# Performance work log

Measured on AMD Instinct MI355X. Metric: run time of the kernel, lower is better.

## Reference

```python
import jax, jax.numpy as jnp
import numpy as np

N_TRAIN, N_TEST, D = 8192, 4096, 16


def setup_inputs() -> dict:
    key = jax.random.key(0)
    k1, k2, k3, k4 = jax.random.split(key, 4)
    train_x = jax.random.normal(k1, (N_TRAIN, D), dtype=jnp.float32)
    train_y = jax.random.normal(k2, (N_TRAIN,), dtype=jnp.float32)
    x = jax.random.normal(k3, (N_TEST, D), dtype=jnp.float32)
    # trained hyperparameters (positive): ScaleKernel outputscale, ARD lengthscales, likelihood noise
    outputscale = jnp.array([0.8], dtype=jnp.float32)
    lengthscale = jax.random.uniform(k4, (D,), dtype=jnp.float32, minval=0.5, maxval=1.5)
    noise = jnp.array([0.05], dtype=jnp.float32)
    return {"train_x": train_x, "train_y": train_y, "x": x,
            "outputscale": outputscale, "lengthscale": lengthscale, "noise": noise}


def _rbf(x1, x2, lengthscale, outputscale):
    # ScaleKernel(RBFKernel(ard)): k(a,b) = s * exp(-0.5 * sum_d ((a_d-b_d)/l_d)^2)
    a = x1 / lengthscale
    b = x2 / lengthscale
    d2 = (jnp.sum(a * a, axis=-1)[:, None]
          + jnp.sum(b * b, axis=-1)[None, :]
          - 2.0 * a @ b.T)
    return outputscale * jnp.exp(-0.5 * jnp.maximum(d2, 0.0))


def reference(train_x, train_y, x, outputscale, lengthscale, noise):
    s = outputscale[0]
    sn = noise[0]
    n = train_x.shape[0]
    # Exact GP posterior with zero mean + Gaussian likelihood:
    # Kxx_hat = K(X,X) + sn*I ; mean = Kxs^T Kxx_hat^{-1} y
    Kxx = _rbf(train_x, train_x, lengthscale, s) + sn * jnp.eye(n, dtype=train_x.dtype)
    L = jnp.linalg.cholesky(Kxx)                       # [N,N]
    Kxs = _rbf(train_x, x, lengthscale, s)             # [N,M]
    alpha = jax.scipy.linalg.cho_solve((L, True), train_y)
    mean = Kxs.T @ alpha                               # [M]
    # predictive variance diag: k(x,x)=s ; var = s - ||L^{-1} Kxs||^2 + noise (likelihood)
    v = jax.scipy.linalg.solve_triangular(L, Kxs, lower=True)  # [N,M]
    var = s - jnp.sum(v * v, axis=0) + sn              # [M]
    return mean, var
```

## Files before the change

### kernel.cpp

```cpp
#include <hip/hip_runtime.h>
#include <stdint.h>


#define N_TRAIN 8192
#define N_TEST  4096
#define DIM     16
#define KDIM    8192
#define CG_ITERS 4
#define NT      (KDIM / 64)

using f32x4  = __attribute__((ext_vector_type(4))) float;
using bf16x8 = __attribute__((ext_vector_type(8))) short;

static __device__ __forceinline__ unsigned short f2bf(float f) {
  unsigned u = __float_as_uint(f);
  u = (u + 0x7FFFu + ((u >> 16) & 1u)) >> 16;
  return (unsigned short)u;
}
static __device__ __forceinline__ float bf2f(unsigned short h) {
  return __uint_as_float(((unsigned)h) << 16);
}

__device__ __forceinline__ void gl_lds16(const void* g, void* l) {
  __builtin_amdgcn_global_load_lds(
      (const __attribute__((address_space(1))) unsigned int*)g,
      (__attribute__((address_space(3))) unsigned int*)l, 16, 0, 0);
}

template <int N>
__device__ __forceinline__ void block_reduceN(float* v, float* sbuf) {
  #pragma unroll
  for (int off = 32; off > 0; off >>= 1)
    #pragma unroll
    for (int i = 0; i < N; ++i) v[i] += __shfl_down(v[i], off);
  int lane = threadIdx.x & 63, w = threadIdx.x >> 6;
  if (lane == 0)
    #pragma unroll
    for (int i = 0; i < N; ++i) sbuf[w * N + i] = v[i];
  __syncthreads();
  #pragma unroll
  for (int i = 0; i < N; ++i)
    v[i] = sbuf[i] + sbuf[N + i] + sbuf[2 * N + i] + sbuf[3 * N + i];
}

__global__ void prep_kernel(const float* __restrict__ tx, const float* __restrict__ xx,
                            const float* __restrict__ ls,
                            float* __restrict__ As, float* __restrict__ an,
                            float* __restrict__ Bs, float* __restrict__ bn) {
  int i = blockIdx.x * 256 + threadIdx.x;
  if (i < N_TRAIN) {
    float s = 0.f;
    #pragma unroll
    for (int d = 0; d < DIM; ++d) {
      float v = tx[(size_t)i * DIM + d] / ls[d];
      As[(size_t)i * DIM + d] = v; s += v * v;
    }
    an[i] = s;
  } else if (i < N_TRAIN + N_TEST) {
    int j = i - N_TRAIN;
    float s = 0.f;
    #pragma unroll
    for (int d = 0; d < DIM; ++d) {
      float v = xx[(size_t)j * DIM + d] / ls[d];
      Bs[(size_t)j * DIM + d] = v; s += v * v;
    }
    bn[j] = s;
  }
}

template <bool DIAG0>
__global__ __launch_bounds__(256) void build_kernel(
    const float* __restrict__ RI, const float* __restrict__ nI,
    const float* __restrict__ RJ, const float* __restrict__ nJ,
    unsigned short* __restrict__ O1,
    const float* __restrict__ osc)
{
  __shared__ float aI[128 * DIM];
  __shared__ float sI[128];
  int t = threadIdx.x;
  int j0 = blockIdx.x * 512, i0 = blockIdx.y * 128;
  for (int e = t; e < 128 * DIM; e += 256) aI[e] = RI[(size_t)i0 * DIM + e];
  if (t < 128) sI[t] = nI[i0 + t];
  __syncthreads();

  int ja = j0 + 2 * t, jb = ja + 1;
  f32x4 aj0[4], aj1[4];
  const f32x4* RJa = (const f32x4*)(RJ + (size_t)ja * DIM);
  const f32x4* RJb = (const f32x4*)(RJ + (size_t)jb * DIM);
  #pragma unroll
  for (int q = 0; q < 4; ++q) { aj0[q] = RJa[q]; aj1[q] = RJb[q]; }
  float nja = nJ[ja], njb = nJ[jb];
  float s = osc[0];

  for (int ic = 0; ic < 128; ic += 2) {
    f32x4 rv[2][4];
    #pragma unroll
    for (int r = 0; r < 2; ++r)
      #pragma unroll
      for (int q = 0; q < 4; ++q)
        rv[r][q] = *(const f32x4*)&aI[(ic + r) * DIM + q * 4];
    #pragma unroll
    for (int r = 0; r < 2; ++r) {
      int i = ic + r;
      float d0 = 0.f, d1 = 0.f;
      #pragma unroll
      for (int q = 0; q < 4; ++q) {
        f32x4 ai = rv[r][q];
        d0 += ai[0]*aj0[q][0] + ai[1]*aj0[q][1] + ai[2]*aj0[q][2] + ai[3]*aj0[q][3];
        d1 += ai[0]*aj1[q][0] + ai[1]*aj1[q][1] + ai[2]*aj1[q][2] + ai[3]*aj1[q][3];
      }
      float d2a = fmaxf(sI[i] + nja - 2.f * d0, 0.f);
      float d2b = fmaxf(sI[i] + njb - 2.f * d1, 0.f);
      float va = s * __expf(-0.5f * d2a);
      float vb = s * __expf(-0.5f * d2b);
      if (DIAG0 && (i0 + i == ja)) va = 0.f;
      if (DIAG0 && (i0 + i == jb)) vb = 0.f;
      unsigned pack = (unsigned)f2bf(va) | ((unsigned)f2bf(vb) << 16);
      *(unsigned*)&O1[(size_t)(i0 + i) * KDIM + ja] = pack;
    }
  }
}


__device__ __forceinline__ void stage_h(const char* gtile, int kbyte,
                                        char* ldsdst, int tid, int wave) {
  #pragma unroll
  for (int q = 0; q < 2; ++q) {
    int o = q * 8192 + tid * 16;
    int r = o >> 7;
    int c = (o & 127) ^ ((r & 7) << 4);
    gl_lds16(gtile + (size_t)r * (KDIM * 2) + kbyte + c,
             ldsdst + q * 8192 + wave * 1024);
  }
}

template <int FINAL>
__global__ __launch_bounds__(512, 1) void gemm256(
    const unsigned short* __restrict__ A,
    const unsigned short* __restrict__ Bm,
    unsigned short* __restrict__ Cq,
    int gy, float* __restrict__ pq)
{
  __shared__ char Ab[2][2][16384];
  __shared__ char Bb[2][2][16384];
  const int tid = threadIdx.x, lane = tid & 63, wave = tid >> 6;
  const int wm = wave >> 2, wn = wave & 3;
  const int nwg = gridDim.x, orig = blockIdx.x;
  const int wgid = (orig & 7) * (nwg >> 3) + (orig >> 3);
  const int bx = wgid / gy, by = wgid % gy;
  const size_t HALF = (size_t)128 * KDIM * 2;

  const char* bA = (const char*)(A  + (size_t)(by * 256) * KDIM);
  const char* bB = (const char*)(Bm + (size_t)(bx * 256) * KDIM);

  const int ar = wm * 64 + (lane & 15);
  const int br = wn * 32 + (lane & 15);
  const int hi = (lane >> 4) * 16;
  int aoff[4][2], boff[2][2];
  #pragma unroll
  for (int mf = 0; mf < 4; ++mf)
    #pragma unroll
    for (int kk = 0; kk < 2; ++kk)
      aoff[mf][kk] = (ar + mf * 16) * 128 + ((hi + kk * 64) ^ ((ar & 7) << 4));
  #pragma unroll
  for (int nf = 0; nf < 2; ++nf)
    #pragma unroll
    for (int kk = 0; kk < 2; ++kk)
      boff[nf][kk] = (br + nf * 16) * 128 + ((hi + kk * 64) ^ ((br & 7) << 4));

  f32x4 acc[2][2][4][2] = {};
  bf16x8 aR[4][2], bR[2][2][2];

#define BAR() __builtin_amdgcn_s_barrier()
#define PRIO1 __builtin_amdgcn_s_setprio(1)
#define PRIO0 __builtin_amdgcn_s_setprio(0)
#define FENCE8() asm volatile("s_waitcnt vmcnt(8)" ::: "memory")
#define FENCE6() asm volatile("s_waitcnt vmcnt(6)" ::: "memory")
#define FENCE0() asm volatile("s_waitcnt vmcnt(0)" ::: "memory")
#define STAGE_A(buf, mh, kb) stage_h(bA + ((mh) ? HALF : 0), kb, &Ab[buf][mh][0], tid, wave)
#define STAGE_B(buf, mh, kb) stage_h(bB + ((mh) ? HALF : 0), kb, &Bb[buf][mh][0], tid, wave)
#define LOAD_A(buf, mh)                                                        \
  { _Pragma("unroll") for (int mf = 0; mf < 4; ++mf)                           \
      _Pragma("unroll") for (int kk = 0; kk < 2; ++kk)                         \
        aR[mf][kk] = *(const bf16x8*)(&Ab[buf][mh][0] + aoff[mf][kk]); }
#define LOAD_B(buf, nh)                                                        \
  { _Pragma("unroll") for (int nf = 0; nf < 2; ++nf)                           \
      _Pragma("unroll") for (int kk = 0; kk < 2; ++kk)                         \
        bR[nh][nf][kk] = *(const bf16x8*)(&Bb[buf][nh][0] + boff[nf][kk]); }
#define MFMA16(mh, nh)                                                         \
  { _Pragma("unroll") for (int kk = 0; kk < 2; ++kk)                           \
      _Pragma("unroll") for (int mf = 0; mf < 4; ++mf)                         \
        _Pragma("unroll") for (int nf = 0; nf < 2; ++nf)                       \
          acc[mh][nh][mf][nf] = __builtin_amdgcn_mfma_f32_16x16x32_bf16(       \
              aR[mf][kk], bR[nh][nf][kk], acc[mh][nh][mf][nf], 0, 0, 0); }

  STAGE_A(0, 0, 0);   STAGE_B(0, 0, 0);   STAGE_B(0, 1, 0);   STAGE_A(0, 1, 0);
  STAGE_A(1, 0, 128); STAGE_B(1, 0, 128); STAGE_B(1, 1, 128); STAGE_A(1, 1, 128);
  FENCE6();
  BAR();

  for (int t = 0; t < NT; t += 2) {
    const bool g = (t + 2 < NT);
    const int kb2 = (t + 2) * 128, kb3 = (t + 3) * 128;
    LOAD_A(0, 0); LOAD_B(0, 0);
    BAR(); PRIO1; MFMA16(0, 0); PRIO0; BAR();
    if (g) STAGE_A(0, 0, kb2);
    LOAD_B(0, 1);
    BAR(); PRIO1; MFMA16(0, 1); PRIO0; BAR();
    if (g) STAGE_B(0, 0, kb2);
    LOAD_A(0, 1);
    BAR(); PRIO1; MFMA16(1, 0); PRIO0; BAR();
    if (g) { STAGE_B(0, 1, kb2); STAGE_A(0, 1, kb2); }
    BAR(); PRIO1; MFMA16(1, 1); PRIO0;
    if (g) { FENCE8(); } else { FENCE0(); }
    BAR();
    LOAD_A(1, 0); LOAD_B(1, 0);
    BAR(); PRIO1; MFMA16(0, 0); PRIO0; BAR();
    if (g) STAGE_A(1, 0, kb3);
    LOAD_B(1, 1);
    BAR(); PRIO1; MFMA16(0, 1); PRIO0; BAR();
    if (g) STAGE_B(1, 0, kb3);
    LOAD_A(1, 1);
    BAR(); PRIO1; MFMA16(1, 0); PRIO0; BAR();
    if (g) { STAGE_B(1, 1, kb3); STAGE_A(1, 1, kb3); }
    BAR(); PRIO1; MFMA16(1, 1); PRIO0;
    if (g) { FENCE6(); }
    BAR();
  }

  const int bm = by * 256, bn = bx * 256;
  if (!FINAL) {
    #pragma unroll
    for (int mh = 0; mh < 2; ++mh)
      #pragma unroll
      for (int nh = 0; nh < 2; ++nh)
        #pragma unroll
        for (int mf = 0; mf < 4; ++mf)
          #pragma unroll
          for (int nf = 0; nf < 2; ++nf) {
            int row = bm + mh * 128 + wm * 64 + mf * 16 + (lane >> 4) * 4;
            int col = bn + nh * 128 + wn * 32 + nf * 16 + (lane & 15);
            #pragma unroll
            for (int rg = 0; rg < 4; ++rg)
              Cq[(size_t)(row + rg) * KDIM + col] = f2bf(acc[mh][nh][mf][nf][rg]);
          }
  } else {
    #pragma unroll
    for (int mh = 0; mh < 2; ++mh)
      #pragma unroll
      for (int mf = 0; mf < 4; ++mf)
        #pragma unroll
        for (int rg = 0; rg < 4; ++rg) {
          int row = bm + mh * 128 + wm * 64 + mf * 16 + (lane >> 4) * 4 + rg;
          float v = 0.f;
          #pragma unroll
          for (int nh = 0; nh < 2; ++nh)
            #pragma unroll
            for (int nf = 0; nf < 2; ++nf) {
              int col = bn + nh * 128 + wn * 32 + nf * 16 + (lane & 15);
              v += acc[mh][nh][mf][nf][rg] * bf2f(A[(size_t)row * KDIM + col]);
            }
          v += __shfl_xor(v, 1); v += __shfl_xor(v, 2);
          v += __shfl_xor(v, 4); v += __shfl_xor(v, 8);
          if ((lane & 15) == 0) atomicAdd(&pq[row], v);
        }
  }
#undef MFMA16
#undef LOAD_B
#undef LOAD_A
#undef STAGE_B
#undef STAGE_A
#undef FENCE0
#undef FENCE6
#undef FENCE8
#undef PRIO0
#undef PRIO1
#undef BAR
}

template <bool FIRST>
__global__ __launch_bounds__(256) void cg_step(
    const unsigned short* __restrict__ Q, unsigned short* __restrict__ R,
    unsigned short* __restrict__ P, const float* __restrict__ y,
    float* __restrict__ scal, float* __restrict__ pq,
    const float* __restrict__ osc, const float* __restrict__ noi)
{
  __shared__ float sbuf[24];
  int c = blockIdx.x, t = threadIdx.x;
  size_t base = (size_t)c * KDIM;
  float dg = osc[0] + noi[0];

  bf16x8 q8[4], r8[4], p8[4];
  #pragma unroll
  for (int k = 0; k < 4; ++k) q8[k] = *(const bf16x8*)&Q[base + k * 2048 + t * 8];
  #pragma unroll
  for (int k = 0; k < 4; ++k) r8[k] = *(const bf16x8*)&R[base + k * 2048 + t * 8];
  if (FIRST) {
    #pragma unroll
    for (int k = 0; k < 4; ++k) p8[k] = r8[k];
  } else {
    #pragma unroll
    for (int k = 0; k < 4; ++k) p8[k] = *(const bf16x8*)&P[base + k * 2048 + t * 8];
  }

  float v[6] = {0.f, 0.f, 0.f, 0.f, 0.f, 0.f};
  #pragma unroll
  for (int k = 0; k < 4; ++k) {
    int j = k * 2048 + t * 8;
    f32x4 ya = *(const f32x4*)&y[j];
    f32x4 yb = *(const f32x4*)&y[j + 4];
    #pragma unroll
    for (int e = 0; e < 8; ++e) {
      float qv = bf2f((unsigned short)q8[k][e]);
      float rv = bf2f((unsigned short)r8[k][e]);
      float yv = (e < 4) ? ya[e] : yb[e - 4];
      if (FIRST) {
        v[0] += rv * qv; v[1] += qv * qv; v[2] += yv * qv;
        v[3] += rv * rv; v[4] += yv * rv;
      } else {
        float pv = bf2f((unsigned short)p8[k][e]);
        v[0] += pv * qv; v[1] += rv * qv; v[2] += qv * qv; v[3] += yv * qv;
        v[4] += pv * pv; v[5] += rv * pv;
      }
    }
  }
  block_reduceN<6>(v, sbuf);

  float rr, yp, yr, mean, bx;
  float pq_od, rq_od, qq_od, yq_od, pp, rp;
  if (FIRST) {
    rr = v[3]; yp = v[4]; yr = v[4]; mean = 0.f; bx = 0.f;
    pq_od = v[0]; rq_od = v[0]; qq_od = v[1]; yq_od = v[2];
    pp = v[3]; rp = v[3];
  } else {
    rr = scal[c*8+0]; yp = scal[c*8+1]; yr = scal[c*8+2];
    mean = scal[c*8+3]; bx = scal[c*8+4];
    pq_od = v[0]; rq_od = v[1]; qq_od = v[2]; yq_od = v[3];
    pp = v[4]; rp = v[5];
  }
  float pAp   = pq_od + dg * pp;
  float rq_e  = rq_od + dg * rp;
  float qq_e  = qq_od + 2.f * dg * pq_od + dg * dg * pp;
  float yq_e  = yq_od + dg * yp;

  float alpha = rr / fmaxf(pAp, 1e-30f);
  mean += alpha * yp;
  bx   += alpha * rr;
  float rrn = fmaxf(rr - 2.f * alpha * rq_e + alpha * alpha * qq_e, 0.f);
  float yrn = yr - alpha * yq_e;
  float beta = rrn / fmaxf(rr, 1e-30f);
  float ypn  = yrn + beta * yp;

  float spp = 0.f;
  #pragma unroll
  for (int k = 0; k < 4; ++k) {
    int j = k * 2048 + t * 8;
    bf16x8 wr, wp;
    #pragma unroll
    for (int e = 0; e < 8; ++e) {
      float pv = bf2f((unsigned short)p8[k][e]);
      float qe = bf2f((unsigned short)q8[k][e]) + dg * pv;
      float rn = bf2f((unsigned short)r8[k][e]) - alpha * qe;
      unsigned short hb = f2bf(rn);
      wr[e] = (short)hb;
      unsigned short hp = f2bf(bf2f(hb) + beta * pv);
      wp[e] = (short)hp;
      float ppv = bf2f(hp);
      spp += ppv * ppv;
    }
    *(bf16x8*)&R[base + j] = wr;
    *(bf16x8*)&P[base + j] = wp;
  }
  __syncthreads();
  float vv[1] = {spp};
  block_reduceN<1>(vv, sbuf);

  if (t == 0) {
    scal[c*8+0] = rrn; scal[c*8+1] = ypn; scal[c*8+2] = yrn;
    scal[c*8+3] = mean; scal[c*8+4] = bx; scal[c*8+5] = vv[0];
    pq[c] = 0.f;
  }
}

__global__ void final_out(float* __restrict__ pq, const float* __restrict__ scal,
                          const float* __restrict__ osc, const float* __restrict__ noi,
                          float* __restrict__ out, int c0, int C)
{
  int c = blockIdx.x * 256 + threadIdx.x;
  if (c >= C) return;
  float dg = osc[0] + noi[0];
  float rr = scal[c*8+0], yp = scal[c*8+1];
  float mean = scal[c*8+3], bx = scal[c*8+4], pp = scal[c*8+5];
  float pAp = pq[c] + dg * pp;
  float alpha = rr / fmaxf(pAp, 1e-30f);
  mean += alpha * yp;
  bx   += alpha * rr;
  out[c0 + c] = mean;
  out[N_TEST + c0 + c] = dg - bx;
  pq[c] = 0.f;
}

extern "C" void kernel_launch(void* const* d_in, const int* in_sizes, int n_in,
                              void* d_out, int out_size, void* d_ws, size_t ws_size,
                              hipStream_t stream) {
  const float* tx = (const float*)d_in[0];
  const float* ty = (const float*)d_in[1];
  const float* xx = (const float*)d_in[2];
  const float* os = (const float*)d_in[3];
  const float* ls = (const float*)d_in[4];
  const float* ns = (const float*)d_in[5];
  float* out = (float*)d_out;
  (void)in_sizes; (void)n_in; (void)out_size;

  auto pad = [](size_t x) { return (x + 255) & ~(size_t)255; };
  size_t fixed = pad((size_t)N_TRAIN * KDIM * 2)
               + pad((size_t)N_TRAIN * DIM * 4) + pad((size_t)N_TRAIN * 4)
               + pad((size_t)N_TEST * DIM * 4) + pad((size_t)N_TEST * 4);
  int C = 4096;
  while (C > 256) {
    size_t tot = fixed + 3 * pad((size_t)C * KDIM * 2)
               + pad((size_t)C * 32) + pad((size_t)C * 4);
    if (tot <= ws_size) break;
    C >>= 1;
  }

  char* w = (char*)d_ws;
  auto alloc = [&](size_t bytes) { char* p = w; w += ((bytes + 255) & ~(size_t)255); return p; };
  unsigned short* Kb = (unsigned short*)alloc((size_t)N_TRAIN * KDIM * 2);
  float* As = (float*)alloc((size_t)N_TRAIN * DIM * 4);
  float* an = (float*)alloc((size_t)N_TRAIN * 4);
  float* Bs = (float*)alloc((size_t)N_TEST * DIM * 4);
  float* bn = (float*)alloc((size_t)N_TEST * 4);
  unsigned short* Rb = (unsigned short*)alloc((size_t)C * KDIM * 2);
  unsigned short* Pb = (unsigned short*)alloc((size_t)C * KDIM * 2);
  unsigned short* Qb = (unsigned short*)alloc((size_t)C * KDIM * 2);
  float* scal = (float*)alloc((size_t)C * 32);
  float* pq   = (float*)alloc((size_t)C * 4);

  prep_kernel<<<48, 256, 0, stream>>>(tx, xx, ls, As, an, Bs, bn);

  build_kernel<true><<<dim3(KDIM / 512, N_TRAIN / 128), 256, 0, stream>>>(
      As, an, As, an, Kb, os);

  for (int c0 = 0; c0 < N_TEST; c0 += C) {
    build_kernel<false><<<dim3(KDIM / 512, C / 128), 256, 0, stream>>>(
        Bs + (size_t)c0 * DIM, bn + c0, As, an, Rb, os);
    int gy = C / 256;
    dim3 gg(32 * gy);
    int scb = (C + 255) / 256;
    for (int it = 0; it < CG_ITERS; ++it) {
      const unsigned short* Ain = (it == 0) ? Rb : Pb;
      int fin = (it == CG_ITERS - 1) ? 1 : 0;
      if (!fin) {
        gemm256<0><<<gg, 512, 0, stream>>>(Ain, Kb, Qb, gy, pq);
        if (it == 0)
          cg_step<true><<<C, 256, 0, stream>>>(Qb, Rb, Pb, ty, scal, pq, os, ns);
        else
          cg_step<false><<<C, 256, 0, stream>>>(Qb, Rb, Pb, ty, scal, pq, os, ns);
      } else {
        gemm256<1><<<gg, 512, 0, stream>>>(Ain, Kb, Qb, gy, pq);
        final_out<<<scb, 256, 0, stream>>>(pq, scal, os, ns, out, c0, C);
      }
    }
  }
}
```

Measured before the change: 1.981 ms.

## Build RBF kernel matrices with bf16 split-precision MFMA and LDS-staged stores

Replaces the scalar FP32 dot-product build kernel with an MFMA version. Each scaled input is split into bf16 hi/lo parts packed so that two 16x16x32 MFMAs approximate the FP32 cross product to about hi*hi+hi*lo+lo*hi accuracy. Results go through an LDS tile and are written out as coalesced 16-byte rows. This targets the cost of building the 8192x8192 and 8192xC kernel matrices. The trade-off is extra prep buffers and slightly reduced dot-product precision.

```diff
diff --git a/kernel.cpp b/kernel.cpp
--- a/kernel.cpp
+++ b/kernel.cpp
@@ -45,15 +45,24 @@
 
 __global__ void prep_kernel(const float* __restrict__ tx, const float* __restrict__ xx,
                             const float* __restrict__ ls,
-                            float* __restrict__ As, float* __restrict__ an,
-                            float* __restrict__ Bs, float* __restrict__ bn) {
+                            unsigned short* __restrict__ TPK,
+                            unsigned short* __restrict__ THH,
+                            unsigned short* __restrict__ TLL,
+                            float* __restrict__ an,
+                            unsigned short* __restrict__ XPK,
+                            float* __restrict__ bn) {
   int i = blockIdx.x * 256 + threadIdx.x;
   if (i < N_TRAIN) {
     float s = 0.f;
     #pragma unroll
     for (int d = 0; d < DIM; ++d) {
       float v = tx[(size_t)i * DIM + d] / ls[d];
-      As[(size_t)i * DIM + d] = v; s += v * v;
+      s += v * v;
+      unsigned short hi = f2bf(v);
+      unsigned short lo = f2bf(v - bf2f(hi));
+      TPK[(size_t)i * 32 + d] = hi;  TPK[(size_t)i * 32 + 16 + d] = lo;
+      THH[(size_t)i * 32 + d] = hi;  THH[(size_t)i * 32 + 16 + d] = hi;
+      TLL[(size_t)i * 32 + d] = lo;  TLL[(size_t)i * 32 + 16 + d] = lo;
     }
     an[i] = s;
   } else if (i < N_TRAIN + N_TEST) {
@@ -62,65 +71,74 @@
     #pragma unroll
     for (int d = 0; d < DIM; ++d) {
       float v = xx[(size_t)j * DIM + d] / ls[d];
-      Bs[(size_t)j * DIM + d] = v; s += v * v;
+      s += v * v;
+      unsigned short hi = f2bf(v);
+      unsigned short lo = f2bf(v - bf2f(hi));
+      XPK[(size_t)j * 32 + d] = hi;  XPK[(size_t)j * 32 + 16 + d] = lo;
     }
     bn[j] = s;
   }
 }
 
+#define TLDS 136
+
 template <bool DIAG0>
-__global__ __launch_bounds__(256) void build_kernel(
-    const float* __restrict__ RI, const float* __restrict__ nI,
-    const float* __restrict__ RJ, const float* __restrict__ nJ,
-    unsigned short* __restrict__ O1,
+__global__ __launch_bounds__(256) void build_mfma(
+    const unsigned short* __restrict__ IPK,
+    const float* __restrict__ nI,
+    const unsigned short* __restrict__ JHH,
+    const unsigned short* __restrict__ JLL,
+    const float* __restrict__ nJ,
+    unsigned short* __restrict__ O,
     const float* __restrict__ osc)
 {
-  __shared__ float aI[128 * DIM];
-  __shared__ float sI[128];
-  int t = threadIdx.x;
-  int j0 = blockIdx.x * 512, i0 = blockIdx.y * 128;
-  for (int e = t; e < 128 * DIM; e += 256) aI[e] = RI[(size_t)i0 * DIM + e];
+  __shared__ unsigned short tile[128 * TLDS];
+  __shared__ float sI[128], sJ[128];
+  int t = threadIdx.x, lane = t & 63, wave = t >> 6;
+  int i0 = blockIdx.y * 128, j0 = blockIdx.x * 128;
   if (t < 128) sI[t] = nI[i0 + t];
+  else         sJ[t - 128] = nJ[j0 + t - 128];
   __syncthreads();
 
-  int ja = j0 + 2 * t, jb = ja + 1;
-  f32x4 aj0[4], aj1[4];
-  const f32x4* RJa = (const f32x4*)(RJ + (size_t)ja * DIM);
-  const f32x4* RJb = (const f32x4*)(RJ + (size_t)jb * DIM);
-  #pragma unroll
-  for (int q = 0; q < 4; ++q) { aj0[q] = RJa[q]; aj1[q] = RJb[q]; }
-  float nja = nJ[ja], njb = nJ[jb];
   float s = osc[0];
-
-  for (int ic = 0; ic < 128; ic += 2) {
-    f32x4 rv[2][4];
-    #pragma unroll
-    for (int r = 0; r < 2; ++r)
+  int ir = lane & 15, ks = lane >> 4;
+
+  bf16x8 af[2];
+  #pragma unroll
+  for (int rt = 0; rt < 2; ++rt)
+    af[rt] = *(const bf16x8*)&IPK[(size_t)(i0 + (wave * 2 + rt) * 16 + ir) * 32 + ks * 8];
+
+  for (int jt = 0; jt < 8; ++jt) {
+    bf16x8 bh = *(const bf16x8*)&JHH[(size_t)(j0 + jt * 16 + ir) * 32 + ks * 8];
+    bf16x8 bl = *(const bf16x8*)&JLL[(size_t)(j0 + jt * 16 + ir) * 32 + ks * 8];
+    f32x4 acc0 = {}, acc1 = {};
+    acc0 = __builtin_amdgcn_mfma_f32_16x16x32_bf16(af[0], bh, acc0, 0, 0, 0);
+    acc0 = __builtin_amdgcn_mfma_f32_16x16x32_bf16(af[0], bl, acc0, 0, 0, 0);
+    acc1 = __builtin_amdgcn_mfma_f32_16x16x32_bf16(af[1], bh, acc1, 0, 0, 0);
+    acc1 = __builtin_amdgcn_mfma_f32_16x16x32_bf16(af[1], bl, acc1, 0, 0, 0);
+    #pragma unroll
+    for (int rt = 0; rt < 2; ++rt) {
+      f32x4 a = rt ? acc1 : acc0;
       #pragma unroll
-      for (int q = 0; q < 4; ++q)
-        rv[r][q] = *(const f32x4*)&aI[(ic + r) * DIM + q * 4];
-    #pragma unroll
-    for (int r = 0; r < 2; ++r) {
-      int i = ic + r;
-      float d0 = 0.f, d1 = 0.f;
-      #pragma unroll
-      for (int q = 0; q < 4; ++q) {
-        f32x4 ai = rv[r][q];
-        d0 += ai[0]*aj0[q][0] + ai[1]*aj0[q][1] + ai[2]*aj0[q][2] + ai[3]*aj0[q][3];
-        d1 += ai[0]*aj1[q][0] + ai[1]*aj1[q][1] + ai[2]*aj1[q][2] + ai[3]*aj1[q][3];
+      for (int rg = 0; rg < 4; ++rg) {
+        int lrow = (wave * 2 + rt) * 16 + ks * 4 + rg;
+        int lcol = jt * 16 + ir;
+        float d2 = fmaxf(sI[lrow] + sJ[lcol] - 2.f * a[rg], 0.f);
+        float v = s * __expf(-0.5f * d2);
+        if (DIAG0 && (i0 + lrow == j0 + lcol)) v = 0.f;
+        tile[lrow * TLDS + lcol] = f2bf(v);
       }
-      float d2a = fmaxf(sI[i] + nja - 2.f * d0, 0.f);
-      float d2b = fmaxf(sI[i] + njb - 2.f * d1, 0.f);
-      float va = s * __expf(-0.5f * d2a);
-      float vb = s * __expf(-0.5f * d2b);
-      if (DIAG0 && (i0 + i == ja)) va = 0.f;
-      if (DIAG0 && (i0 + i == jb)) vb = 0.f;
-      unsigned pack = (unsigned)f2bf(va) | ((unsigned)f2bf(vb) << 16);
-      *(unsigned*)&O1[(size_t)(i0 + i) * KDIM + ja] = pack;
-    }
-  }
-}
-
+    }
+  }
+  __syncthreads();
+  #pragma unroll
+  for (int pass = 0; pass < 8; ++pass) {
+    int r = pass * 16 + (t >> 4);
+    int cb = (t & 15) * 8;
+    *(bf16x8*)&O[(size_t)(i0 + r) * KDIM + j0 + cb] =
+        *(const bf16x8*)&tile[r * TLDS + cb];
+  }
+}
 
 __device__ __forceinline__ void stage_h(const char* gtile, int kbyte,
                                         char* ldsdst, int tid, int wave) {
@@ -414,8 +432,8 @@
 
   auto pad = [](size_t x) { return (x + 255) & ~(size_t)255; };
   size_t fixed = pad((size_t)N_TRAIN * KDIM * 2)
-               + pad((size_t)N_TRAIN * DIM * 4) + pad((size_t)N_TRAIN * 4)
-               + pad((size_t)N_TEST * DIM * 4) + pad((size_t)N_TEST * 4);
+               + 3 * pad((size_t)N_TRAIN * 64) + pad((size_t)N_TRAIN * 4)
+               + pad((size_t)N_TEST * 64) + pad((size_t)N_TEST * 4);
   int C = 4096;
   while (C > 256) {
     size_t tot = fixed + 3 * pad((size_t)C * KDIM * 2)
@@ -426,10 +444,12 @@
 
   char* w = (char*)d_ws;
   auto alloc = [&](size_t bytes) { char* p = w; w += ((bytes + 255) & ~(size_t)255); return p; };
-  unsigned short* Kb = (unsigned short*)alloc((size_t)N_TRAIN * KDIM * 2);
-  float* As = (float*)alloc((size_t)N_TRAIN * DIM * 4);
+  unsigned short* Kb  = (unsigned short*)alloc((size_t)N_TRAIN * KDIM * 2);
+  unsigned short* TPK = (unsigned short*)alloc((size_t)N_TRAIN * 64);
+  unsigned short* THH = (unsigned short*)alloc((size_t)N_TRAIN * 64);
+  unsigned short* TLL = (unsigned short*)alloc((size_t)N_TRAIN * 64);
   float* an = (float*)alloc((size_t)N_TRAIN * 4);
-  float* Bs = (float*)alloc((size_t)N_TEST * DIM * 4);
+  unsigned short* XPK = (unsigned short*)alloc((size_t)N_TEST * 64);
   float* bn = (float*)alloc((size_t)N_TEST * 4);
   unsigned short* Rb = (unsigned short*)alloc((size_t)C * KDIM * 2);
   unsigned short* Pb = (unsigned short*)alloc((size_t)C * KDIM * 2);
@@ -437,14 +457,14 @@
   float* scal = (float*)alloc((size_t)C * 32);
   float* pq   = (float*)alloc((size_t)C * 4);
 
-  prep_kernel<<<48, 256, 0, stream>>>(tx, xx, ls, As, an, Bs, bn);
-
-  build_kernel<true><<<dim3(KDIM / 512, N_TRAIN / 128), 256, 0, stream>>>(
-      As, an, As, an, Kb, os);
+  prep_kernel<<<48, 256, 0, stream>>>(tx, xx, ls, TPK, THH, TLL, an, XPK, bn);
+
+  build_mfma<true><<<dim3(KDIM / 128, N_TRAIN / 128), 256, 0, stream>>>(
+      TPK, an, THH, TLL, an, Kb, os);
 
   for (int c0 = 0; c0 < N_TEST; c0 += C) {
-    build_kernel<false><<<dim3(KDIM / 512, C / 128), 256, 0, stream>>>(
-        Bs + (size_t)c0 * DIM, bn + c0, As, an, Rb, os);
+    build_mfma<false><<<dim3(KDIM / 128, C / 128), 256, 0, stream>>>(
+        XPK + (size_t)c0 * 32, bn + c0, THH, TLL, an, Rb, os);
     int gy = C / 256;
     dim3 gg(32 * gy);
     int scb = (C + 255) / 256;
```

After: 1.930 ms. -2.6%, faster.
